# Kernel optimization log

Hardware: AMD Instinct MI355X
Metric: run time of the kernel (lower is better)

Reference implementation:

```python
import jax, jax.numpy as jnp
import numpy as np

B, N, D = 4, 4096, 128
LOSS_WEIGHT = 1.0  # module hardcodes self.loss_weight = 1.0


def setup_inputs() -> dict:
    key = jax.random.key(0)
    k1, k2 = jax.random.split(key)
    corr_pred = jax.random.normal(k1, (B, N, D), dtype=jnp.float32)
    corr_target = jax.random.normal(k2, (B, N, D), dtype=jnp.float32)
    return {"corr_pred": corr_pred, "corr_target": corr_target}


def chamfer_distance(x, y):
    # x: [B, N, D], y: [B, N, D]
    x2 = jnp.sum(x * x, axis=-1)                      # [B, N]  diag of x @ x^T
    y2 = jnp.sum(y * y, axis=-1)                      # [B, N]  diag of y @ y^T
    zz = jnp.einsum('bnd,bmd->bnm', x, y)             # [B, N, N]
    # P[b,i,j] = ||x_i||^2 + ||y_j||^2 - 2 x_i . y_j
    P = x2[:, :, None] + y2[:, None, :] - 2.0 * zz
    P = jnp.clip(P, 0.0, 100.0)
    return jnp.mean(jnp.min(P, axis=1)) + jnp.mean(jnp.min(P, axis=2))


def reference(corr_pred, corr_target):
    chamfer = chamfer_distance(corr_pred, corr_target)
    return LOSS_WEIGHT * chamfer / corr_target.shape[0]
```

## Files before the change

### kernel.cpp

```cpp
#include <hip/hip_runtime.h>
#include <hip/hip_bf16.h>

#define B_ 4
#define N_ 4096
#define D_ 128
#define EPB (N_ * D_)
#define COFF 1024.0f

typedef float f32x4 __attribute__((ext_vector_type(4)));
typedef int   int8v __attribute__((ext_vector_type(8)));
typedef int   int4v __attribute__((ext_vector_type(4)));

#define SQRT2 1.41421356237309515f


__global__ __launch_bounds__(256) void prep_kernel(
    const float* __restrict__ X, const float* __restrict__ Y,
    unsigned char* __restrict__ Xb, unsigned char* __restrict__ Yb,
    float* __restrict__ x2, float* __restrict__ y2,
    int* __restrict__ rowmin, int* __restrict__ colmin)
{
    const int which = blockIdx.y;
    const float* __restrict__ src = which ? Y : X;
    unsigned char* __restrict__ dst = which ? Yb : Xb;
    float* __restrict__ nrm = which ? y2 : x2;
    int* __restrict__ mn = which ? colmin : rowmin;

    const int t = threadIdx.x;
    const int r = t & 15, c = t >> 4;
    const int rgG = blockIdx.x;
    const int row = rgG * 16 + r;

    const float4 v0 = *(const float4*)(src + (size_t)row * D_ + c * 8);
    const float4 v1 = *(const float4*)(src + (size_t)row * D_ + c * 8 + 4);

    float sq = v0.x * v0.x;
    sq = fmaf(v0.y, v0.y, sq); sq = fmaf(v0.z, v0.z, sq); sq = fmaf(v0.w, v0.w, sq);
    sq = fmaf(v1.x, v1.x, sq); sq = fmaf(v1.y, v1.y, sq);
    sq = fmaf(v1.z, v1.z, sq); sq = fmaf(v1.w, v1.w, sq);

    unsigned lo = 0, hi = 0;
    lo = __builtin_amdgcn_cvt_pk_fp8_f32(v0.x * SQRT2, v0.y * SQRT2, lo, false);
    lo = __builtin_amdgcn_cvt_pk_fp8_f32(v0.z * SQRT2, v0.w * SQRT2, lo, true);
    hi = __builtin_amdgcn_cvt_pk_fp8_f32(v1.x * SQRT2, v1.y * SQRT2, hi, false);
    hi = __builtin_amdgcn_cvt_pk_fp8_f32(v1.z * SQRT2, v1.w * SQRT2, hi, true);

    const int b = row >> 12;
    const int rg = (row & (N_ - 1)) >> 4;
    uint2 packed; packed.x = lo; packed.y = hi;
    *(uint2*)(dst + (size_t)b * EPB + rg * 2048 + (c >> 2) * 512
              + r * 32 + (c & 3) * 8) = packed;

    __shared__ float s[256];
    s[r * 16 + c] = sq;
    __syncthreads();
    if (t < 16) {
        const float4* sp = (const float4*)(s + t * 16);
        float4 a = sp[0], bq = sp[1], cq = sp[2], d = sp[3];
        float tot = a.x + a.y + a.z + a.w + bq.x + bq.y + bq.z + bq.w
                  + cq.x + cq.y + cq.z + cq.w + d.x + d.y + d.z + d.w;
        nrm[rgG * 16 + t] = tot;
        mn[rgG * 16 + t] = 0x7f7fffff;
    }
}

__global__ __launch_bounds__(256, 2) void chamfer_mfma(
    const unsigned char* __restrict__ Xb, const unsigned char* __restrict__ Yb,
    const float* __restrict__ x2, const float* __restrict__ y2,
    int* __restrict__ rowmin, int* __restrict__ colmin)
{
    const int b = blockIdx.z;
    const int iT = blockIdx.y;
    const int jc = blockIdx.x;
    const int tid = threadIdx.x;
    const int wave = tid >> 6, lane = tid & 63;
    const int quad = lane >> 4, l16 = lane & 15;
    const int rowBase = iT * 256 + wave * 64;

    const unsigned char* __restrict__ Xp = Xb + (size_t)b * EPB;
    const unsigned char* __restrict__ Yp = Yb + (size_t)b * EPB;

    int8v af[4];
    #pragma unroll
    for (int rt = 0; rt < 4; rt++) {
        const unsigned char* ap = Xp + ((rowBase >> 4) + rt) * 2048
                                 + quad * 512 + l16 * 32;
        const int4v lo = *(const int4v*)(ap);
        const int4v hi = *(const int4v*)(ap + 16);
        af[rt] = (int8v){lo.x, lo.y, lo.z, lo.w, hi.x, hi.y, hi.z, hi.w};
    }
    float x2v[4][4];
    #pragma unroll
    for (int rt = 0; rt < 4; rt++)
        #pragma unroll
        for (int i = 0; i < 4; i++)
            x2v[rt][i] = x2[(size_t)b * N_ + rowBase + rt * 16 + quad * 4 + i];

    float rmin[4][4];
    #pragma unroll
    for (int rt = 0; rt < 4; rt++)
        #pragma unroll
        for (int i = 0; i < 4; i++) rmin[rt][i] = 3.0e38f;

    for (int s = 0; s < 4; ++s) {
        const int colBase = jc * 256 + s * 64;
        const int cg = colBase >> 4;

        float y2v[4];
        #pragma unroll
        for (int ct = 0; ct < 4; ct++)
            y2v[ct] = y2[(size_t)b * N_ + colBase + ct * 16 + l16];

        int8v bfv[4];
        #pragma unroll
        for (int ct = 0; ct < 4; ct++) {
            const unsigned char* bp = Yp + (size_t)(cg + ct) * 2048
                                     + quad * 512 + l16 * 32;
            const int4v lo = *(const int4v*)(bp);
            const int4v hi = *(const int4v*)(bp + 16);
            bfv[ct] = (int8v){lo.x, lo.y, lo.z, lo.w, hi.x, hi.y, hi.z, hi.w};
        }

        f32x4 acc[4][4];
        #pragma unroll
        for (int i = 0; i < 4; i++)
            #pragma unroll
            for (int j = 0; j < 4; j++)
                acc[i][j] = (f32x4){0.f, 0.f, 0.f, 0.f};

        #pragma unroll
        for (int rt = 0; rt < 4; rt++)
            #pragma unroll
            for (int ct = 0; ct < 4; ct++)
                acc[rt][ct] = __builtin_amdgcn_mfma_scale_f32_16x16x128_f8f6f4(
                    af[rt], bfv[ct], acc[rt][ct],
                    0, 0,
                    0, 127,
                    0, 127);

        float cmin[4];
        #pragma unroll
        for (int ct = 0; ct < 4; ct++) cmin[ct] = 3.0e38f;
        #pragma unroll
        for (int rt = 0; rt < 4; rt++)
            #pragma unroll
            for (int i = 0; i < 4; i++) {
                const float xv = x2v[rt][i];
                float rm = rmin[rt][i];
                #pragma unroll
                for (int ct = 0; ct < 4; ct++) {
                    const float a = acc[rt][ct][i];
                    rm = fminf(rm, y2v[ct] - a);
                    cmin[ct] = fminf(cmin[ct], xv - a);
                }
                rmin[rt][i] = rm;
            }
        #pragma unroll
        for (int ct = 0; ct < 4; ct++) {
            float v = cmin[ct];
            v = fminf(v, __shfl_xor(v, 16));
            v = fminf(v, __shfl_xor(v, 32));
            if (quad == 0)
                atomicMin(&colmin[(size_t)b * N_ + colBase + ct * 16 + l16],
                          __float_as_int(v + COFF));
        }
    }

    #pragma unroll
    for (int rt = 0; rt < 4; rt++)
        #pragma unroll
        for (int i = 0; i < 4; i++) {
            float v = rmin[rt][i];
            #pragma unroll
            for (int m = 1; m < 16; m <<= 1) v = fminf(v, __shfl_xor(v, m));
            if (l16 == 0) {
                float c = fminf(fmaxf(x2v[rt][i] + v, 0.0f), 100.0f);
                atomicMin(&rowmin[(size_t)b * N_ + rowBase + rt * 16 + quad * 4 + i],
                          __float_as_int(c));
            }
        }
}

__global__ __launch_bounds__(1024) void finalize_kernel(
    const int* __restrict__ rowmin, const int* __restrict__ colmin,
    const float* __restrict__ y2, float* __restrict__ out)
{
    float s = 0.f;
    for (int i = threadIdx.x; i < B_ * N_ / 4; i += 1024) {
        int4 v = ((const int4*)rowmin)[i];
        s += __int_as_float(v.x) + __int_as_float(v.y) +
             __int_as_float(v.z) + __int_as_float(v.w);
        int4 c = ((const int4*)colmin)[i];
        float4 yv = ((const float4*)y2)[i];
        s += fminf(fmaxf(__int_as_float(c.x) - COFF + yv.x, 0.f), 100.f);
        s += fminf(fmaxf(__int_as_float(c.y) - COFF + yv.y, 0.f), 100.f);
        s += fminf(fmaxf(__int_as_float(c.z) - COFF + yv.z, 0.f), 100.f);
        s += fminf(fmaxf(__int_as_float(c.w) - COFF + yv.w, 0.f), 100.f);
    }
    #pragma unroll
    for (int m = 1; m < 64; m <<= 1) s += __shfl_xor(s, m);
    __shared__ float sm[16];
    if ((threadIdx.x & 63) == 0) sm[threadIdx.x >> 6] = s;
    __syncthreads();
    if (threadIdx.x == 0) {
        float t = 0.f;
        #pragma unroll
        for (int i = 0; i < 16; i++) t += sm[i];
        out[0] = t / ((float)B_ * (float)N_) / (float)B_;
    }
}

extern "C" void kernel_launch(void* const* d_in, const int* in_sizes, int n_in,
                              void* d_out, int out_size, void* d_ws, size_t ws_size,
                              hipStream_t stream) {
    const float* X = (const float*)d_in[0];
    const float* Y = (const float*)d_in[1];

    char* ws = (char*)d_ws;
    const size_t f8_bytes = (size_t)B_ * N_ * D_;
    unsigned char* Xb = (unsigned char*)ws;
    unsigned char* Yb = (unsigned char*)(ws + f8_bytes);
    char* ws2 = ws + 2 * f8_bytes;
    const size_t vec_bytes = (size_t)B_ * N_ * 4;
    float* x2     = (float*)(ws2);
    float* y2     = (float*)(ws2 + vec_bytes);
    int*   rowmin = (int*)  (ws2 + 2 * vec_bytes);
    int*   colmin = (int*)  (ws2 + 3 * vec_bytes);
    float* out = (float*)d_out;

    prep_kernel<<<dim3(B_ * N_ / 16, 2), 256, 0, stream>>>(
        X, Y, Xb, Yb, x2, y2, rowmin, colmin);
    chamfer_mfma<<<dim3(16, N_ / 256, B_), 256, 0, stream>>>(
        Xb, Yb, x2, y2, rowmin, colmin);
    finalize_kernel<<<1, 1024, 0, stream>>>(rowmin, colmin, y2, out);
}
```

Before: 91.21 us.

## Fuse finalize into chamfer kernel via last-block counter and prefetch Y tiles

Removes the separate finalize launch: each chamfer block bumps a global counter after its atomics, and the last block to finish performs the final reduction and writes the output. The chamfer main loop now double-buffers the FP8 Y fragments, loading the next column tile while the MFMAs run on the current one, and loads all y2 norms up front. The prep kernel swaps its thread mapping so the per-row norm reduction uses wave shuffles instead of shared memory and a barrier. The cost is more registers in the chamfer kernel, which could lower occupancy, plus a serialized tail reduction done by a single 256-thread block.

```diff
diff --git a/kernel.cpp b/kernel.cpp
--- a/kernel.cpp
+++ b/kernel.cpp
@@ -6,6 +6,7 @@
 #define D_ 128
 #define EPB (N_ * D_)
 #define COFF 1024.0f
+#define NBLK (16 * 16 * B_)
 
 typedef float f32x4 __attribute__((ext_vector_type(4)));
 typedef int   int8v __attribute__((ext_vector_type(8)));
@@ -18,7 +19,8 @@
     const float* __restrict__ X, const float* __restrict__ Y,
     unsigned char* __restrict__ Xb, unsigned char* __restrict__ Yb,
     float* __restrict__ x2, float* __restrict__ y2,
-    int* __restrict__ rowmin, int* __restrict__ colmin)
+    int* __restrict__ rowmin, int* __restrict__ colmin,
+    int* __restrict__ counter)
 {
     const int which = blockIdx.y;
     const float* __restrict__ src = which ? Y : X;
@@ -27,9 +29,11 @@
     int* __restrict__ mn = which ? colmin : rowmin;
 
     const int t = threadIdx.x;
-    const int r = t & 15, c = t >> 4;
+    const int r = t >> 4, c = t & 15;
     const int rgG = blockIdx.x;
     const int row = rgG * 16 + r;
+
+    if (which == 0 && rgG == 0 && t == 0) *counter = 0;
 
     const float4 v0 = *(const float4*)(src + (size_t)row * D_ + c * 8);
     const float4 v1 = *(const float4*)(src + (size_t)row * D_ + c * 8 + 4);
@@ -38,6 +42,8 @@
     sq = fmaf(v0.y, v0.y, sq); sq = fmaf(v0.z, v0.z, sq); sq = fmaf(v0.w, v0.w, sq);
     sq = fmaf(v1.x, v1.x, sq); sq = fmaf(v1.y, v1.y, sq);
     sq = fmaf(v1.z, v1.z, sq); sq = fmaf(v1.w, v1.w, sq);
+    #pragma unroll
+    for (int m = 1; m < 16; m <<= 1) sq += __shfl_xor(sq, m);
 
     unsigned lo = 0, hi = 0;
     lo = __builtin_amdgcn_cvt_pk_fp8_f32(v0.x * SQRT2, v0.y * SQRT2, lo, false);
@@ -51,23 +57,17 @@
     *(uint2*)(dst + (size_t)b * EPB + rg * 2048 + (c >> 2) * 512
               + r * 32 + (c & 3) * 8) = packed;
 
-    __shared__ float s[256];
-    s[r * 16 + c] = sq;
-    __syncthreads();
-    if (t < 16) {
-        const float4* sp = (const float4*)(s + t * 16);
-        float4 a = sp[0], bq = sp[1], cq = sp[2], d = sp[3];
-        float tot = a.x + a.y + a.z + a.w + bq.x + bq.y + bq.z + bq.w
-                  + cq.x + cq.y + cq.z + cq.w + d.x + d.y + d.z + d.w;
-        nrm[rgG * 16 + t] = tot;
-        mn[rgG * 16 + t] = 0x7f7fffff;
+    if (c == 0) {
+        nrm[row] = sq;
+        mn[row] = 0x7f7fffff;
     }
 }
 
 __global__ __launch_bounds__(256, 2) void chamfer_mfma(
     const unsigned char* __restrict__ Xb, const unsigned char* __restrict__ Yb,
     const float* __restrict__ x2, const float* __restrict__ y2,
-    int* __restrict__ rowmin, int* __restrict__ colmin)
+    int* __restrict__ rowmin, int* __restrict__ colmin,
+    int* __restrict__ counter, float* __restrict__ out)
 {
     const int b = blockIdx.z;
     const int iT = blockIdx.y;
@@ -96,29 +96,43 @@
         for (int i = 0; i < 4; i++)
             x2v[rt][i] = x2[(size_t)b * N_ + rowBase + rt * 16 + quad * 4 + i];
 
+    float y2all[16];
+    #pragma unroll
+    for (int idx = 0; idx < 16; idx++)
+        y2all[idx] = y2[(size_t)b * N_ + jc * 256 + idx * 16 + l16];
+
     float rmin[4][4];
     #pragma unroll
     for (int rt = 0; rt < 4; rt++)
         #pragma unroll
         for (int i = 0; i < 4; i++) rmin[rt][i] = 3.0e38f;
 
+    int8v bfv[2][4];
+    #pragma unroll
+    for (int ct = 0; ct < 4; ct++) {
+        const unsigned char* bp = Yp + (size_t)((jc * 256) >> 4 << 11)
+                                 + ct * 2048 + quad * 512 + l16 * 32;
+        const int4v lo = *(const int4v*)(bp);
+        const int4v hi = *(const int4v*)(bp + 16);
+        bfv[0][ct] = (int8v){lo.x, lo.y, lo.z, lo.w, hi.x, hi.y, hi.z, hi.w};
+    }
+
+    #pragma unroll
     for (int s = 0; s < 4; ++s) {
+        const int cur = s & 1;
         const int colBase = jc * 256 + s * 64;
-        const int cg = colBase >> 4;
-
-        float y2v[4];
-        #pragma unroll
-        for (int ct = 0; ct < 4; ct++)
-            y2v[ct] = y2[(size_t)b * N_ + colBase + ct * 16 + l16];
-
-        int8v bfv[4];
-        #pragma unroll
-        for (int ct = 0; ct < 4; ct++) {
-            const unsigned char* bp = Yp + (size_t)(cg + ct) * 2048
-                                     + quad * 512 + l16 * 32;
-            const int4v lo = *(const int4v*)(bp);
-            const int4v hi = *(const int4v*)(bp + 16);
-            bfv[ct] = (int8v){lo.x, lo.y, lo.z, lo.w, hi.x, hi.y, hi.z, hi.w};
+
+        if (s < 3) {
+            const int cgn = (jc * 256 + (s + 1) * 64) >> 4;
+            #pragma unroll
+            for (int ct = 0; ct < 4; ct++) {
+                const unsigned char* bp = Yp + (size_t)(cgn + ct) * 2048
+                                         + quad * 512 + l16 * 32;
+                const int4v lo = *(const int4v*)(bp);
+                const int4v hi = *(const int4v*)(bp + 16);
+                bfv[cur ^ 1][ct] = (int8v){lo.x, lo.y, lo.z, lo.w,
+                                           hi.x, hi.y, hi.z, hi.w};
+            }
         }
 
         f32x4 acc[4][4];
@@ -133,7 +147,7 @@
             #pragma unroll
             for (int ct = 0; ct < 4; ct++)
                 acc[rt][ct] = __builtin_amdgcn_mfma_scale_f32_16x16x128_f8f6f4(
-                    af[rt], bfv[ct], acc[rt][ct],
+                    af[rt], bfv[cur][ct], acc[rt][ct],
                     0, 0,
                     0, 127,
                     0, 127);
@@ -150,7 +164,7 @@
                 #pragma unroll
                 for (int ct = 0; ct < 4; ct++) {
                     const float a = acc[rt][ct][i];
-                    rm = fminf(rm, y2v[ct] - a);
+                    rm = fminf(rm, y2all[s * 4 + ct] - a);
                     cmin[ct] = fminf(cmin[ct], xv - a);
                 }
                 rmin[rt][i] = rm;
@@ -179,14 +193,18 @@
                           __float_as_int(c));
             }
         }
-}
-
-__global__ __launch_bounds__(1024) void finalize_kernel(
-    const int* __restrict__ rowmin, const int* __restrict__ colmin,
-    const float* __restrict__ y2, float* __restrict__ out)
-{
+
+    __threadfence();
+    __shared__ int isLast;
+    __syncthreads();
+    if (tid == 0)
+        isLast = (atomicAdd(counter, 1) == NBLK - 1);
+    __syncthreads();
+    if (!isLast) return;
+    __threadfence();
+
     float s = 0.f;
-    for (int i = threadIdx.x; i < B_ * N_ / 4; i += 1024) {
+    for (int i = tid; i < B_ * N_ / 4; i += 256) {
         int4 v = ((const int4*)rowmin)[i];
         s += __int_as_float(v.x) + __int_as_float(v.y) +
              __int_as_float(v.z) + __int_as_float(v.w);
@@ -199,15 +217,12 @@
     }
     #pragma unroll
     for (int m = 1; m < 64; m <<= 1) s += __shfl_xor(s, m);
-    __shared__ float sm[16];
-    if ((threadIdx.x & 63) == 0) sm[threadIdx.x >> 6] = s;
+    __shared__ float sm[4];
+    if ((tid & 63) == 0) sm[tid >> 6] = s;
     __syncthreads();
-    if (threadIdx.x == 0) {
-        float t = 0.f;
-        #pragma unroll
-        for (int i = 0; i < 16; i++) t += sm[i];
-        out[0] = t / ((float)B_ * (float)N_) / (float)B_;
-    }
+    if (tid == 0)
+        out[0] = (sm[0] + sm[1] + sm[2] + sm[3])
+                 / ((float)B_ * (float)N_) / (float)B_;
 }
 
 extern "C" void kernel_launch(void* const* d_in, const int* in_sizes, int n_in,
@@ -222,15 +237,15 @@
     unsigned char* Yb = (unsigned char*)(ws + f8_bytes);
     char* ws2 = ws + 2 * f8_bytes;
     const size_t vec_bytes = (size_t)B_ * N_ * 4;
-    float* x2     = (float*)(ws2);
-    float* y2     = (float*)(ws2 + vec_bytes);
-    int*   rowmin = (int*)  (ws2 + 2 * vec_bytes);
-    int*   colmin = (int*)  (ws2 + 3 * vec_bytes);
+    float* x2      = (float*)(ws2);
+    float* y2      = (float*)(ws2 + vec_bytes);
+    int*   rowmin  = (int*)  (ws2 + 2 * vec_bytes);
+    int*   colmin  = (int*)  (ws2 + 3 * vec_bytes);
+    int*   counter = (int*)  (ws2 + 4 * vec_bytes);
     float* out = (float*)d_out;
 
     prep_kernel<<<dim3(B_ * N_ / 16, 2), 256, 0, stream>>>(
-        X, Y, Xb, Yb, x2, y2, rowmin, colmin);
+        X, Y, Xb, Yb, x2, y2, rowmin, colmin, counter);
     chamfer_mfma<<<dim3(16, N_ / 256, B_), 256, 0, stream>>>(
-        Xb, Yb, x2, y2, rowmin, colmin);
-    finalize_kernel<<<1, 1024, 0, stream>>>(rowmin, colmin, y2, out);
+        Xb, Yb, x2, y2, rowmin, colmin, counter, out);
 }
```

New measurement: 213.2 us. 134% more time.
